# Optimization experiments

Measured on AMD Instinct MI355X. Metric: run time of the kernel, lower is better.

## Reference

```python
import jax, jax.numpy as jnp
import numpy as np

B, S, E, Q, A = 32, 2048, 1024, 1024, 512

def setup_inputs() -> dict:
    key = jax.random.key(0)
    k1, k2, k3, k4, k5 = jax.random.split(key, 5)
    scale = lambda d: 1.0 / np.sqrt(d)
    return {
        "inputs": jax.random.normal(k1, (B, S, E), dtype=jnp.float32),
        "query": jax.random.normal(k2, (B, Q), dtype=jnp.float32),
        "W_in": jax.random.normal(k3, (E, A), dtype=jnp.float32) * scale(E),
        "W_q": jax.random.normal(k4, (Q, A), dtype=jnp.float32) * scale(Q),
        "w_att": jax.random.normal(k5, (A,), dtype=jnp.float32) * scale(A),
    }

def reference(inputs, query, W_in, W_q, w_att):
    # projected inputs: [B, S, A]
    proj_in = jnp.einsum("bse,ea->bsa", inputs, W_in)
    # projected query, broadcast over S: [B, 1, A]
    proj_q = (query @ W_q)[:, None, :]
    # additive scores: [B, S]
    scores = jnp.einsum("bsa,a->bs", jnp.tanh(proj_in + proj_q), w_att)
    weights = jax.nn.softmax(scores, axis=1)  # over sequence dim
    # context over PROJECTED inputs (as in original): [B, A]
    context = jnp.einsum("bs,bsa->ba", weights, proj_in)
    return context
```

## Files before the change

### kernel.cpp

```cpp
#include <hip/hip_runtime.h>
#include <hip/hip_fp16.h>
#include <cstdint>
#include <cstddef>

#define Bb 32
#define Ss 2048
#define Ee 1024
#define Qq 1024
#define Aa 512

typedef _Float16 half8 __attribute__((ext_vector_type(8)));
typedef float f32x4 __attribute__((ext_vector_type(4)));

#define WS_PROJQ 0u
#define WS_MPART 65536u
#define WS_LPART 67584u
#define WS_CTXP  69632u
#define WS_WWS   1118208u

__device__ __forceinline__ float fast_tanh(float x) {
  float e = __expf(2.0f * x);
  return 1.0f - __fdividef(2.0f, e + 1.0f);
}

__global__ void k_convw(const float* __restrict__ win, _Float16* __restrict__ wws) {
  int gid = blockIdx.x * 256 + threadIdx.x;
  int a  = gid & 511;
  int ks = (gid >> 9) & 3;
  int kt = gid >> 11;
  int k0 = kt * 32 + ks * 8;
  half8 v;
  #pragma unroll
  for (int j = 0; j < 8; ++j) v[j] = (_Float16)win[(size_t)(k0 + j) * Aa + a];
  *(half8*)(wws + ((size_t)kt * 16384 + (size_t)ks * 4096 + (size_t)a * 8)) = v;
}

__global__ void k_projq(const float* __restrict__ query, const float* __restrict__ wq,
                        float* __restrict__ projq) {
  __shared__ float red[256];
  int b  = blockIdx.y;
  int al = threadIdx.x & 63;
  int eq = threadIdx.x >> 6;
  int a  = blockIdx.x * 64 + al;
  const float* q = query + (size_t)b * Qq;
  float s = 0.f;
  int e0 = eq * 256;
  #pragma unroll 4
  for (int e = e0; e < e0 + 256; ++e)
    s += q[e] * wq[(size_t)e * Aa + a];
  red[threadIdx.x] = s;
  __syncthreads();
  if (eq == 0)
    projq[(size_t)b * Aa + a] = red[al] + red[al + 64] + red[al + 128] + red[al + 192];
}

__global__ __launch_bounds__(512, 2)
void k_main(const float* __restrict__ inp, const _Float16* __restrict__ wws,
            const float* __restrict__ projq, const float* __restrict__ watt,
            float* __restrict__ mpart, float* __restrict__ lpart,
            float* __restrict__ ctxp)
{
  __shared__ __align__(16) _Float16 Alds[2][4 * 128 * 8];
  __shared__ float pq_s[512];
  __shared__ float wa_s[512];
  __shared__ float sc4[128][4];
  __shared__ float pbuf[128];
  __shared__ float redv[8];
  __shared__ float ctx2[2][512];

  const int tid = threadIdx.x;
  const int l   = tid & 63;
  const int w   = tid >> 6;
  const int lr  = l & 15;
  const int kb  = l >> 4;
  const int wr  = w >> 2;
  const int wc  = w & 3;
  const int b   = blockIdx.y;
  const int ch  = blockIdx.x;

  pq_s[tid] = projq[(size_t)b * Aa + tid];
  wa_s[tid] = watt[tid];

  const int arow = w * 16 + lr;
  const float* arow_ptr = inp + ((size_t)(b * Ss + ch * 128 + arow)) * Ee + kb * 8;
  const int aoff = (kb * 128 + arow) * 8;

  f32x4 acc[4][8];
  #pragma unroll
  for (int m = 0; m < 4; ++m)
    #pragma unroll
    for (int n = 0; n < 8; ++n) acc[m][n] = (f32x4){0.f, 0.f, 0.f, 0.f};

  const half8* Bg = (const half8*)wws + (size_t)kb * 512 + wc * 128 + lr;

  {
    float4 f0 = *(const float4*)(arow_ptr);
    float4 f1 = *(const float4*)(arow_ptr + 4);
    half8 h;
    h[0]=(_Float16)f0.x; h[1]=(_Float16)f0.y; h[2]=(_Float16)f0.z; h[3]=(_Float16)f0.w;
    h[4]=(_Float16)f1.x; h[5]=(_Float16)f1.y; h[6]=(_Float16)f1.z; h[7]=(_Float16)f1.w;
    *(half8*)(Alds[0] + aoff) = h;
  }
  __syncthreads();

  int p = 0;
  for (int kt = 0; kt < 32; ++kt) {
    float4 f0, f1;
    if (kt < 31) {
      const float* pp = arow_ptr + (size_t)(kt + 1) * 32;
      f0 = *(const float4*)(pp);
      f1 = *(const float4*)(pp + 4);
    }
    half8 bf[8];
    const half8* Bk = Bg + (size_t)kt * 2048;
    #pragma unroll
    for (int n = 0; n < 8; ++n) bf[n] = Bk[n * 16];
    half8 af[4];
    #pragma unroll
    for (int m = 0; m < 4; ++m)
      af[m] = *(const half8*)(Alds[p] + (kb * 128 + wr * 64 + m * 16 + lr) * 8);
    #pragma unroll
    for (int m = 0; m < 4; ++m)
      #pragma unroll
      for (int n = 0; n < 8; ++n)
        acc[m][n] = __builtin_amdgcn_mfma_f32_16x16x32_f16(af[m], bf[n], acc[m][n], 0, 0, 0);
    if (kt < 31) {
      half8 h;
      h[0]=(_Float16)f0.x; h[1]=(_Float16)f0.y; h[2]=(_Float16)f0.z; h[3]=(_Float16)f0.w;
      h[4]=(_Float16)f1.x; h[5]=(_Float16)f1.y; h[6]=(_Float16)f1.z; h[7]=(_Float16)f1.w;
      *(half8*)(Alds[p ^ 1] + aoff) = h;
    }
    __syncthreads();
    p ^= 1;
  }

  float sp[4][4];
  #pragma unroll
  for (int m = 0; m < 4; ++m)
    #pragma unroll
    for (int j = 0; j < 4; ++j) sp[m][j] = 0.f;

  #pragma unroll
  for (int n = 0; n < 8; ++n) {
    int col = wc * 128 + n * 16 + lr;
    float wan = wa_s[col], pqn = pq_s[col];
    #pragma unroll
    for (int m = 0; m < 4; ++m)
      #pragma unroll
      for (int j = 0; j < 4; ++j)
        sp[m][j] += fast_tanh(acc[m][n][j] + pqn) * wan;
  }
  #pragma unroll
  for (int m = 0; m < 4; ++m)
    #pragma unroll
    for (int j = 0; j < 4; ++j) {
      float v = sp[m][j];
      v += __shfl_xor(v, 1);
      v += __shfl_xor(v, 2);
      v += __shfl_xor(v, 4);
      v += __shfl_xor(v, 8);
      sp[m][j] = v;
    }
  if (lr == 0) {
    #pragma unroll
    for (int m = 0; m < 4; ++m)
      #pragma unroll
      for (int j = 0; j < 4; ++j)
        sc4[wr * 64 + m * 16 + kb * 4 + j][wc] = sp[m][j];
  }
  __syncthreads();

  if (tid < 128) {
    float s = sc4[tid][0] + sc4[tid][1] + sc4[tid][2] + sc4[tid][3];
    pbuf[tid] = s;
    float mx = s;
    #pragma unroll
    for (int off = 1; off < 64; off <<= 1) mx = fmaxf(mx, __shfl_xor(mx, off));
    if (l == 0) redv[w] = mx;
  }
  __syncthreads();
  float Mx = fmaxf(redv[0], redv[1]);
  if (tid < 128) {
    float pe = __expf(pbuf[tid] - Mx);
    pbuf[tid] = pe;
    float ls = pe;
    #pragma unroll
    for (int off = 1; off < 64; off <<= 1) ls += __shfl_xor(ls, off);
    if (l == 0) redv[4 + w] = ls;
  }
  __syncthreads();

  float cv[8];
  #pragma unroll
  for (int n = 0; n < 8; ++n) cv[n] = 0.f;
  #pragma unroll
  for (int m = 0; m < 4; ++m)
    #pragma unroll
    for (int j = 0; j < 4; ++j) {
      float pw = pbuf[wr * 64 + m * 16 + kb * 4 + j];
      #pragma unroll
      for (int n = 0; n < 8; ++n) cv[n] += pw * acc[m][n][j];
    }
  #pragma unroll
  for (int n = 0; n < 8; ++n) {
    float v = cv[n];
    v += __shfl_xor(v, 16);
    v += __shfl_xor(v, 32);
    cv[n] = v;
  }
  if (l < 16) {
    #pragma unroll
    for (int n = 0; n < 8; ++n) ctx2[wr][wc * 128 + n * 16 + lr] = cv[n];
  }
  __syncthreads();

  int pi = b * 16 + ch;
  ctxp[(size_t)pi * 512 + tid] = ctx2[0][tid] + ctx2[1][tid];
  if (tid == 0) { mpart[pi] = Mx; lpart[pi] = redv[4] + redv[5]; }
}

__global__ void k_comb(const float* __restrict__ mpart, const float* __restrict__ lpart,
                       const float* __restrict__ ctxp, float* __restrict__ out) {
  int b = blockIdx.x, a = threadIdx.x;
  float Mg = -1e30f;
  #pragma unroll
  for (int i = 0; i < 16; ++i) Mg = fmaxf(Mg, mpart[b * 16 + i]);
  float den = 0.f, s = 0.f;
  #pragma unroll
  for (int i = 0; i < 16; ++i) {
    float e = __expf(mpart[b * 16 + i] - Mg);
    den += lpart[b * 16 + i] * e;
    s   += ctxp[((size_t)(b * 16 + i)) * 512 + a] * e;
  }
  out[(size_t)b * 512 + a] = s / den;
}

extern "C" void kernel_launch(void* const* d_in, const int* in_sizes, int n_in,
                              void* d_out, int out_size, void* d_ws, size_t ws_size,
                              hipStream_t stream) {
  const float* inputs = (const float*)d_in[0];
  const float* query  = (const float*)d_in[1];
  const float* W_in   = (const float*)d_in[2];
  const float* W_q    = (const float*)d_in[3];
  const float* w_att  = (const float*)d_in[4];
  float* out = (float*)d_out;

  char* ws = (char*)d_ws;
  float*    projq = (float*)(ws + WS_PROJQ);
  float*    mpart = (float*)(ws + WS_MPART);
  float*    lpart = (float*)(ws + WS_LPART);
  float*    ctxp  = (float*)(ws + WS_CTXP);
  _Float16* wws   = (_Float16*)(ws + WS_WWS);

  k_convw<<<256, 256, 0, stream>>>(W_in, wws);
  k_projq<<<dim3(8, 32), 256, 0, stream>>>(query, W_q, projq);
  k_main<<<dim3(16, 32), 512, 0, stream>>>(inputs, wws, projq, w_att, mpart, lpart, ctxp);
  k_comb<<<32, 512, 0, stream>>>(mpart, lpart, ctxp, out);
}
```

Before: 167.9 us.

## Stage W_in tiles in double-buffered LDS instead of per-wave global loads

```diff
diff --git a/kernel.cpp b/kernel.cpp
--- a/kernel.cpp
+++ b/kernel.cpp
@@ -61,6 +61,7 @@
             float* __restrict__ ctxp)
 {
   __shared__ __align__(16) _Float16 Alds[2][4 * 128 * 8];
+  __shared__ __align__(16) _Float16 Blds[2][4 * 512 * 8];
   __shared__ float pq_s[512];
   __shared__ float wa_s[512];
   __shared__ float sc4[128][4];
@@ -85,50 +86,70 @@
   const float* arow_ptr = inp + ((size_t)(b * Ss + ch * 128 + arow)) * Ee + kb * 8;
   const int aoff = (kb * 128 + arow) * 8;
 
+  const char* bbase = (const char*)wws + (size_t)tid * 16;
+  const int boff = tid * 16;
+
   f32x4 acc[4][8];
   #pragma unroll
   for (int m = 0; m < 4; ++m)
     #pragma unroll
     for (int n = 0; n < 8; ++n) acc[m][n] = (f32x4){0.f, 0.f, 0.f, 0.f};
-
-  const half8* Bg = (const half8*)wws + (size_t)kb * 512 + wc * 128 + lr;
 
   {
     float4 f0 = *(const float4*)(arow_ptr);
     float4 f1 = *(const float4*)(arow_ptr + 4);
+    float4 g0 = *(const float4*)(bbase);
+    float4 g1 = *(const float4*)(bbase + 8192);
+    float4 g2 = *(const float4*)(bbase + 16384);
+    float4 g3 = *(const float4*)(bbase + 24576);
     half8 h;
     h[0]=(_Float16)f0.x; h[1]=(_Float16)f0.y; h[2]=(_Float16)f0.z; h[3]=(_Float16)f0.w;
     h[4]=(_Float16)f1.x; h[5]=(_Float16)f1.y; h[6]=(_Float16)f1.z; h[7]=(_Float16)f1.w;
     *(half8*)(Alds[0] + aoff) = h;
+    char* bd = (char*)Blds[0] + boff;
+    *(float4*)(bd)         = g0;
+    *(float4*)(bd + 8192)  = g1;
+    *(float4*)(bd + 16384) = g2;
+    *(float4*)(bd + 24576) = g3;
   }
   __syncthreads();
 
   int p = 0;
   for (int kt = 0; kt < 32; ++kt) {
-    float4 f0, f1;
-    if (kt < 31) {
-      const float* pp = arow_ptr + (size_t)(kt + 1) * 32;
-      f0 = *(const float4*)(pp);
-      f1 = *(const float4*)(pp + 4);
-    }
-    half8 bf[8];
-    const half8* Bk = Bg + (size_t)kt * 2048;
-    #pragma unroll
-    for (int n = 0; n < 8; ++n) bf[n] = Bk[n * 16];
-    half8 af[4];
+    const int ktn = (kt < 31) ? kt + 1 : 31;
+    const float* ap = arow_ptr + (size_t)ktn * 32;
+    float4 f0 = *(const float4*)(ap);
+    float4 f1 = *(const float4*)(ap + 4);
+    const char* bs = bbase + (size_t)ktn * 32768;
+    float4 g0 = *(const float4*)(bs);
+    float4 g1 = *(const float4*)(bs + 8192);
+    float4 g2 = *(const float4*)(bs + 16384);
+    float4 g3 = *(const float4*)(bs + 24576);
+
+    half8 af[4], bf[8];
     #pragma unroll
     for (int m = 0; m < 4; ++m)
       af[m] = *(const half8*)(Alds[p] + (kb * 128 + wr * 64 + m * 16 + lr) * 8);
+    #pragma unroll
+    for (int n = 0; n < 8; ++n)
+      bf[n] = *(const half8*)(Blds[p] + (kb * 512 + wc * 128 + n * 16 + lr) * 8);
+
     #pragma unroll
     for (int m = 0; m < 4; ++m)
       #pragma unroll
       for (int n = 0; n < 8; ++n)
         acc[m][n] = __builtin_amdgcn_mfma_f32_16x16x32_f16(af[m], bf[n], acc[m][n], 0, 0, 0);
+
     if (kt < 31) {
       half8 h;
       h[0]=(_Float16)f0.x; h[1]=(_Float16)f0.y; h[2]=(_Float16)f0.z; h[3]=(_Float16)f0.w;
       h[4]=(_Float16)f1.x; h[5]=(_Float16)f1.y; h[6]=(_Float16)f1.z; h[7]=(_Float16)f1.w;
       *(half8*)(Alds[p ^ 1] + aoff) = h;
+      char* bd = (char*)Blds[p ^ 1] + boff;
+      *(float4*)(bd)         = g0;
+      *(float4*)(bd + 8192)  = g1;
+      *(float4*)(bd + 16384) = g2;
+      *(float4*)(bd + 24576) = g3;
     }
     __syncthreads();
     p ^= 1;
```

Result: slower. 171.4 us (+2.1%).

## Shrink main-kernel tile to 32 rows with 256 threads and 64 chunks per batch

Applied to the files above, without the earlier changes.

```diff
diff --git a/kernel.cpp b/kernel.cpp
--- a/kernel.cpp
+++ b/kernel.cpp
@@ -14,9 +14,9 @@
 
 #define WS_PROJQ 0u
 #define WS_MPART 65536u
-#define WS_LPART 67584u
-#define WS_CTXP  69632u
-#define WS_WWS   1118208u
+#define WS_LPART 73728u
+#define WS_CTXP  81920u
+#define WS_WWS   4276224u
 
 __device__ __forceinline__ float fast_tanh(float x) {
   float e = __expf(2.0f * x);
@@ -54,48 +54,48 @@
     projq[(size_t)b * Aa + a] = red[al] + red[al + 64] + red[al + 128] + red[al + 192];
 }
 
-__global__ __launch_bounds__(512, 2)
+__global__ __launch_bounds__(256, 4)
 void k_main(const float* __restrict__ inp, const _Float16* __restrict__ wws,
             const float* __restrict__ projq, const float* __restrict__ watt,
             float* __restrict__ mpart, float* __restrict__ lpart,
             float* __restrict__ ctxp)
 {
-  __shared__ __align__(16) _Float16 Alds[2][4 * 128 * 8];
+  __shared__ __align__(16) _Float16 Alds[2][4 * 32 * 8];
   __shared__ float pq_s[512];
   __shared__ float wa_s[512];
-  __shared__ float sc4[128][4];
-  __shared__ float pbuf[128];
-  __shared__ float redv[8];
-  __shared__ float ctx2[2][512];
+  __shared__ float sc4[32][4];
+  __shared__ float pbuf[32];
 
   const int tid = threadIdx.x;
   const int l   = tid & 63;
   const int w   = tid >> 6;
   const int lr  = l & 15;
   const int kb  = l >> 4;
-  const int wr  = w >> 2;
-  const int wc  = w & 3;
   const int b   = blockIdx.y;
   const int ch  = blockIdx.x;
 
-  pq_s[tid] = projq[(size_t)b * Aa + tid];
-  wa_s[tid] = watt[tid];
-
-  const int arow = w * 16 + lr;
-  const float* arow_ptr = inp + ((size_t)(b * Ss + ch * 128 + arow)) * Ee + kb * 8;
-  const int aoff = (kb * 128 + arow) * 8;
-
-  f32x4 acc[4][8];
-  #pragma unroll
-  for (int m = 0; m < 4; ++m)
+  pq_s[tid]       = projq[(size_t)b * Aa + tid];
+  pq_s[tid + 256] = projq[(size_t)b * Aa + tid + 256];
+  wa_s[tid]       = watt[tid];
+  wa_s[tid + 256] = watt[tid + 256];
+
+  const bool astage = (tid < 128);
+  const int kbs  = (tid >> 5) & 3;
+  const int rows = tid & 31;
+  const float* asrc = inp + ((size_t)(b * Ss + ch * 32 + rows)) * Ee + kbs * 8;
+  const int aoff = (kbs * 32 + rows) * 8;
+
+  const half8* Bg = (const half8*)wws + (size_t)kb * 512 + w * 128 + lr;
+
+  f32x4 acc[2][8];
+  #pragma unroll
+  for (int m = 0; m < 2; ++m)
     #pragma unroll
     for (int n = 0; n < 8; ++n) acc[m][n] = (f32x4){0.f, 0.f, 0.f, 0.f};
 
-  const half8* Bg = (const half8*)wws + (size_t)kb * 512 + wc * 128 + lr;
-
-  {
-    float4 f0 = *(const float4*)(arow_ptr);
-    float4 f1 = *(const float4*)(arow_ptr + 4);
+  if (astage) {
+    float4 f0 = *(const float4*)(asrc);
+    float4 f1 = *(const float4*)(asrc + 4);
     half8 h;
     h[0]=(_Float16)f0.x; h[1]=(_Float16)f0.y; h[2]=(_Float16)f0.z; h[3]=(_Float16)f0.w;
     h[4]=(_Float16)f1.x; h[5]=(_Float16)f1.y; h[6]=(_Float16)f1.z; h[7]=(_Float16)f1.w;
@@ -106,25 +106,39 @@
   int p = 0;
   for (int kt = 0; kt < 32; ++kt) {
     float4 f0, f1;
-    if (kt < 31) {
-      const float* pp = arow_ptr + (size_t)(kt + 1) * 32;
-      f0 = *(const float4*)(pp);
-      f1 = *(const float4*)(pp + 4);
-    }
-    half8 bf[8];
+    if (astage) {
+      const int ktn = (kt < 31) ? kt + 1 : 31;
+      const float* ap = asrc + (size_t)ktn * 32;
+      f0 = *(const float4*)(ap);
+      f1 = *(const float4*)(ap + 4);
+    }
+
     const half8* Bk = Bg + (size_t)kt * 2048;
-    #pragma unroll
-    for (int n = 0; n < 8; ++n) bf[n] = Bk[n * 16];
-    half8 af[4];
-    #pragma unroll
-    for (int m = 0; m < 4; ++m)
-      af[m] = *(const half8*)(Alds[p] + (kb * 128 + wr * 64 + m * 16 + lr) * 8);
-    #pragma unroll
-    for (int m = 0; m < 4; ++m)
-      #pragma unroll
-      for (int n = 0; n < 8; ++n)
-        acc[m][n] = __builtin_amdgcn_mfma_f32_16x16x32_f16(af[m], bf[n], acc[m][n], 0, 0, 0);
-    if (kt < 31) {
+    half8 bf0 = Bk[0], bf1 = Bk[16], bf2 = Bk[32], bf3 = Bk[48];
+
+    half8 af0 = *(const half8*)(Alds[p] + (kb * 32 +      lr) * 8);
+    half8 af1 = *(const half8*)(Alds[p] + (kb * 32 + 16 + lr) * 8);
+
+    acc[0][0] = __builtin_amdgcn_mfma_f32_16x16x32_f16(af0, bf0, acc[0][0], 0, 0, 0);
+    acc[1][0] = __builtin_amdgcn_mfma_f32_16x16x32_f16(af1, bf0, acc[1][0], 0, 0, 0);
+    acc[0][1] = __builtin_amdgcn_mfma_f32_16x16x32_f16(af0, bf1, acc[0][1], 0, 0, 0);
+    acc[1][1] = __builtin_amdgcn_mfma_f32_16x16x32_f16(af1, bf1, acc[1][1], 0, 0, 0);
+    acc[0][2] = __builtin_amdgcn_mfma_f32_16x16x32_f16(af0, bf2, acc[0][2], 0, 0, 0);
+    acc[1][2] = __builtin_amdgcn_mfma_f32_16x16x32_f16(af1, bf2, acc[1][2], 0, 0, 0);
+    acc[0][3] = __builtin_amdgcn_mfma_f32_16x16x32_f16(af0, bf3, acc[0][3], 0, 0, 0);
+    acc[1][3] = __builtin_amdgcn_mfma_f32_16x16x32_f16(af1, bf3, acc[1][3], 0, 0, 0);
+
+    half8 bf4 = Bk[64], bf5 = Bk[80], bf6 = Bk[96], bf7 = Bk[112];
+    acc[0][4] = __builtin_amdgcn_mfma_f32_16x16x32_f16(af0, bf4, acc[0][4], 0, 0, 0);
+    acc[1][4] = __builtin_amdgcn_mfma_f32_16x16x32_f16(af1, bf4, acc[1][4], 0, 0, 0);
+    acc[0][5] = __builtin_amdgcn_mfma_f32_16x16x32_f16(af0, bf5, acc[0][5], 0, 0, 0);
+    acc[1][5] = __builtin_amdgcn_mfma_f32_16x16x32_f16(af1, bf5, acc[1][5], 0, 0, 0);
+    acc[0][6] = __builtin_amdgcn_mfma_f32_16x16x32_f16(af0, bf6, acc[0][6], 0, 0, 0);
+    acc[1][6] = __builtin_amdgcn_mfma_f32_16x16x32_f16(af1, bf6, acc[1][6], 0, 0, 0);
+    acc[0][7] = __builtin_amdgcn_mfma_f32_16x16x32_f16(af0, bf7, acc[0][7], 0, 0, 0);
+    acc[1][7] = __builtin_amdgcn_mfma_f32_16x16x32_f16(af1, bf7, acc[1][7], 0, 0, 0);
+
+    if (astage && kt < 31) {
       half8 h;
       h[0]=(_Float16)f0.x; h[1]=(_Float16)f0.y; h[2]=(_Float16)f0.z; h[3]=(_Float16)f0.w;
       h[4]=(_Float16)f1.x; h[5]=(_Float16)f1.y; h[6]=(_Float16)f1.z; h[7]=(_Float16)f1.w;
@@ -134,24 +148,24 @@
     p ^= 1;
   }
 
-  float sp[4][4];
-  #pragma unroll
-  for (int m = 0; m < 4; ++m)
+  float sp[2][4];
+  #pragma unroll
+  for (int m = 0; m < 2; ++m)
     #pragma unroll
     for (int j = 0; j < 4; ++j) sp[m][j] = 0.f;
 
   #pragma unroll
   for (int n = 0; n < 8; ++n) {
-    int col = wc * 128 + n * 16 + lr;
+    int col = w * 128 + n * 16 + lr;
     float wan = wa_s[col], pqn = pq_s[col];
     #pragma unroll
-    for (int m = 0; m < 4; ++m)
+    for (int m = 0; m < 2; ++m)
       #pragma unroll
       for (int j = 0; j < 4; ++j)
         sp[m][j] += fast_tanh(acc[m][n][j] + pqn) * wan;
   }
   #pragma unroll
-  for (int m = 0; m < 4; ++m)
+  for (int m = 0; m < 2; ++m)
     #pragma unroll
     for (int j = 0; j < 4; ++j) {
       float v = sp[m][j];
@@ -163,30 +177,25 @@
     }
   if (lr == 0) {
     #pragma unroll
-    for (int m = 0; m < 4; ++m)
+    for (int m = 0; m < 2; ++m)
       #pragma unroll
       for (int j = 0; j < 4; ++j)
-        sc4[wr * 64 + m * 16 + kb * 4 + j][wc] = sp[m][j];
-  }
-  __syncthreads();
-
-  if (tid < 128) {
+        sc4[m * 16 + kb * 4 + j][w] = sp[m][j];
+  }
+  __syncthreads();
+
+  const int pi = b * 64 + ch;
+  if (tid < 32) {
     float s = sc4[tid][0] + sc4[tid][1] + sc4[tid][2] + sc4[tid][3];
-    pbuf[tid] = s;
     float mx = s;
     #pragma unroll
-    for (int off = 1; off < 64; off <<= 1) mx = fmaxf(mx, __shfl_xor(mx, off));
-    if (l == 0) redv[w] = mx;
-  }
-  __syncthreads();
-  float Mx = fmaxf(redv[0], redv[1]);
-  if (tid < 128) {
-    float pe = __expf(pbuf[tid] - Mx);
+    for (int off = 1; off < 32; off <<= 1) mx = fmaxf(mx, __shfl_xor(mx, off));
+    float pe = __expf(s - mx);
+    float ls = pe;
+    #pragma unroll
+    for (int off = 1; off < 32; off <<= 1) ls += __shfl_xor(ls, off);
     pbuf[tid] = pe;
-    float ls = pe;
-    #pragma unroll
-    for (int off = 1; off < 64; off <<= 1) ls += __shfl_xor(ls, off);
-    if (l == 0) redv[4 + w] = ls;
+    if (tid == 0) { mpart[pi] = mx; lpart[pi] = ls; }
   }
   __syncthreads();
 
@@ -194,10 +203,10 @@
   #pragma unroll
   for (int n = 0; n < 8; ++n) cv[n] = 0.f;
   #pragma unroll
-  for (int m = 0; m < 4; ++m)
+  for (int m = 0; m < 2; ++m)
     #pragma unroll
     for (int j = 0; j < 4; ++j) {
-      float pw = pbuf[wr * 64 + m * 16 + kb * 4 + j];
+      float pw = pbuf[m * 16 + kb * 4 + j];
       #pragma unroll
       for (int n = 0; n < 8; ++n) cv[n] += pw * acc[m][n][j];
     }
@@ -210,27 +219,23 @@
   }
   if (l < 16) {
     #pragma unroll
-    for (int n = 0; n < 8; ++n) ctx2[wr][wc * 128 + n * 16 + lr] = cv[n];
-  }
-  __syncthreads();
-
-  int pi = b * 16 + ch;
-  ctxp[(size_t)pi * 512 + tid] = ctx2[0][tid] + ctx2[1][tid];
-  if (tid == 0) { mpart[pi] = Mx; lpart[pi] = redv[4] + redv[5]; }
+    for (int n = 0; n < 8; ++n)
+      ctxp[(size_t)pi * 512 + w * 128 + n * 16 + l] = cv[n];
+  }
 }
 
 __global__ void k_comb(const float* __restrict__ mpart, const float* __restrict__ lpart,
                        const float* __restrict__ ctxp, float* __restrict__ out) {
   int b = blockIdx.x, a = threadIdx.x;
   float Mg = -1e30f;
-  #pragma unroll
-  for (int i = 0; i < 16; ++i) Mg = fmaxf(Mg, mpart[b * 16 + i]);
+  #pragma unroll 8
+  for (int i = 0; i < 64; ++i) Mg = fmaxf(Mg, mpart[b * 64 + i]);
   float den = 0.f, s = 0.f;
-  #pragma unroll
-  for (int i = 0; i < 16; ++i) {
-    float e = __expf(mpart[b * 16 + i] - Mg);
-    den += lpart[b * 16 + i] * e;
-    s   += ctxp[((size_t)(b * 16 + i)) * 512 + a] * e;
+  #pragma unroll 8
+  for (int i = 0; i < 64; ++i) {
+    float e = __expf(mpart[b * 64 + i] - Mg);
+    den += lpart[b * 64 + i] * e;
+    s   += ctxp[((size_t)(b * 64 + i)) * 512 + a] * e;
   }
   out[(size_t)b * 512 + a] = s / den;
 }
@@ -254,6 +259,6 @@
 
   k_convw<<<256, 256, 0, stream>>>(W_in, wws);
   k_projq<<<dim3(8, 32), 256, 0, stream>>>(query, W_q, projq);
-  k_main<<<dim3(16, 32), 512, 0, stream>>>(inputs, wws, projq, w_att, mpart, lpart, ctxp);
+  k_main<<<dim3(64, 32), 256, 0, stream>>>(inputs, wws, projq, w_att, mpart, lpart, ctxp);
   k_comb<<<32, 512, 0, stream>>>(mpart, lpart, ctxp, out);
 }
```

New measurement: 195.4 us. +16.4%, slower.
